# Kernel tuning notes

Measured on AMD Instinct MI355X. Metric: run time of the kernel, lower is better.

The kernel has to match this reference:

```python
import jax, jax.numpy as jnp
import numpy as np

B, S, PATCH_DIM, TRANS_DIM, POS_HID = 16, 4096, 384, 384, 128
SCALE = TRANS_DIM ** (-0.5)

def gelu(x):
    return jax.nn.gelu(x, approximate=False)  # torch nn.GELU default = exact erf

def setup_inputs() -> dict:
    key = jax.random.key(0)
    ks = jax.random.split(key, 16)
    def lin(k, fan_in, shape):
        bound = 1.0 / np.sqrt(fan_in)
        return jax.random.uniform(k, shape, jnp.float32, -bound, bound)
    return {
        "idx": 0,
        "q": jax.random.normal(ks[0], (B, S, TRANS_DIM), jnp.float32),
        "x": jax.random.normal(ks[1], (B, S, 3 + PATCH_DIM), jnp.float32),
        "W_pos1": lin(ks[2], 3, (3, POS_HID)),
        "b_pos1": lin(ks[3], 3, (POS_HID,)),
        "W_pos2": lin(ks[4], POS_HID, (POS_HID, TRANS_DIM)),
        "b_pos2": lin(ks[5], POS_HID, (TRANS_DIM,)),
        "W_in": lin(ks[6], PATCH_DIM, (PATCH_DIM, TRANS_DIM)),
        "b_in": lin(ks[7], PATCH_DIM, (TRANS_DIM,)),
        "W_q": lin(ks[8], TRANS_DIM, (TRANS_DIM, TRANS_DIM)),
        "W_k": lin(ks[9], TRANS_DIM, (TRANS_DIM, TRANS_DIM)),
        "W_v": lin(ks[10], TRANS_DIM, (TRANS_DIM, TRANS_DIM)),
        "W_g1": lin(ks[11], TRANS_DIM, (TRANS_DIM, TRANS_DIM)),
        "b_g1": lin(ks[12], TRANS_DIM, (TRANS_DIM,)),
        "W_g2": lin(ks[13], TRANS_DIM, (TRANS_DIM, TRANS_DIM)),
        "b_g2": lin(ks[14], TRANS_DIM, (TRANS_DIM,)),
        "W_out": lin(ks[15], TRANS_DIM, (TRANS_DIM, PATCH_DIM)),
        "b_out": jnp.zeros((PATCH_DIM,), jnp.float32),
    }

def reference(idx, q, x, W_pos1, b_pos1, W_pos2, b_pos2, W_in, b_in,
              W_q, W_k, W_v, W_g1, b_g1, W_g2, b_g2, W_out, b_out):
    centroid = x[:, :, :3]          # [B,S,3]
    pre = x[:, :, 3:]               # [B,S,patch_dim]
    pos_emb = gelu(centroid @ W_pos1 + b_pos1) @ W_pos2 + b_pos2
    h = pre @ W_in + b_in + pos_emb  # [B,S,trans_dim]
    # idx == 0 path: q = w_qs(h)
    q_out = h @ W_q
    k = h @ W_k
    v = h @ W_v
    gate = gelu((q_out - k) @ W_g1 + b_g1) @ W_g2 + b_g2
    attn = jax.nn.softmax(gate * SCALE, axis=-1)  # softmax over channel dim
    res = (attn * v) @ W_out + b_out + pre
    return (q_out, res)
```

## Files before the change

### kernel.cpp

```cpp
#include <hip/hip_runtime.h>


#define NTOK   65536
#define DIMS   384
#define XC     387
#define TM     32
#define LDP    392
#define PHP    136
#define SCALE  0.051031036307982884f
#define WS_WEIGHT_ELEMS 1081344
#define WS_FLAG_OFF     (WS_WEIGHT_ELEMS)

typedef __bf16 bf16x8 __attribute__((ext_vector_type(8)));
typedef float  floatx4 __attribute__((ext_vector_type(4)));

__device__ __forceinline__ float bf2f(ushort u) {
    return __uint_as_float(((unsigned)u) << 16);
}
__device__ __forceinline__ ushort f2bf(float f) {
    unsigned u = __float_as_uint(f);
    unsigned r = (u + 0x7FFFu + ((u >> 16) & 1u)) >> 16;
    return (ushort)r;
}
__device__ __forceinline__ float gelu_f(float v) {
    return 0.5f * v * (1.0f + erff(v * 0.70710678118654752f));
}
__device__ __forceinline__ float ldg(const void* p, size_t i, int isbf) {
    return isbf ? bf2f(((const ushort*)p)[i]) : ((const float*)p)[i];
}
__device__ __forceinline__ void stg(void* p, size_t i, float v, int isbf) {
    if (isbf) ((ushort*)p)[i] = f2bf(v);
    else      ((float*)p)[i]  = v;
}

__global__ void detect_dtype(const ushort* x, int* flag) {
    int ok = 1;
    for (int i = threadIdx.x; i < 256; i += 64) {
        ushort u = x[2 * i];
        int e = (u >> 7) & 0xFF;
        if (!(e == 0 || (e >= 90 && e <= 141))) ok = 0;
    }
    unsigned long long m = __ballot(ok);
    if (threadIdx.x == 0) *flag = (m == ~0ULL) ? 1 : 0;
}

__global__ void prep_weights(
    const void* __restrict__ Wpos2, const void* __restrict__ Win,
    const void* __restrict__ Wq,    const void* __restrict__ Wk,
    const void* __restrict__ Wv,    const void* __restrict__ Wg1,
    const void* __restrict__ Wg2,   const void* __restrict__ Wo,
    ushort* __restrict__ ws, const int* __restrict__ flagp)
{
    const int isbf = *flagp;
    const int nt   = blockIdx.x;
    const int y    = blockIdx.y;
    const int lane = threadIdx.x;
    const void* src;
    int kt, KT; size_t dstoff;
    if (y < 4) { src = Wpos2; KT = 4; kt = y; dstoff = 0; }
    else {
        int wi = (y - 4) / 12; kt = (y - 4) % 12; KT = 12;
        const void* tab[7] = {Win, Wq, Wk, Wv, Wg1, Wg2, Wo};
        src = tab[wi];
        dstoff = 49152 + (size_t)wi * 147456;
    }
    const int k = kt * 32 + (lane >> 4) * 8;
    const int n = nt * 16 + (lane & 15);
    ushort* dst = ws + dstoff + ((size_t)(nt * KT + kt) * 64 + lane) * 8;
    if (isbf) {
        const ushort* s16 = (const ushort*)src;
#pragma unroll
        for (int j = 0; j < 8; ++j) dst[j] = s16[(size_t)(k + j) * 384 + n];
    } else {
        const float* s32 = (const float*)src;
#pragma unroll
        for (int j = 0; j < 8; ++j) dst[j] = f2bf(s32[(size_t)(k + j) * 384 + n]);
    }
}

template<int KT, int LDA>
__device__ __forceinline__ void gemm_acc(const ushort* sA, const bf16x8* wq,
                                         int ntBase, int lane, floatx4 acc[2][3])
{
    const int l16 = lane & 15, quad = lane >> 4;
#pragma unroll
    for (int kt = 0; kt < KT; ++kt) {
        const int k = kt * 32 + quad * 8;
        bf16x8 a[2];
#pragma unroll
        for (int mt = 0; mt < 2; ++mt)
            a[mt] = *reinterpret_cast<const bf16x8*>(sA + (mt * 16 + l16) * LDA + k);
        bf16x8 b[3];
#pragma unroll
        for (int i = 0; i < 3; ++i)
            b[i] = wq[((size_t)(ntBase + i) * KT + kt) * 64 + lane];
#pragma unroll
        for (int mt = 0; mt < 2; ++mt)
#pragma unroll
            for (int i = 0; i < 3; ++i)
                acc[mt][i] = __builtin_amdgcn_mfma_f32_16x16x32_bf16(a[mt], b[i], acc[mt][i], 0, 0, 0);
    }
}

__device__ __forceinline__ void zero_acc(floatx4 acc[2][3]) {
#pragma unroll
    for (int mt = 0; mt < 2; ++mt)
#pragma unroll
        for (int i = 0; i < 3; ++i)
            acc[mt][i] = (floatx4){0.f, 0.f, 0.f, 0.f};
}

__device__ __forceinline__ void bias_acc(floatx4 acc[2][3], const void* b,
                                         int ntBase, int l16, int isbf) {
#pragma unroll
    for (int i = 0; i < 3; ++i) {
        float bv = ldg(b, (ntBase + i) * 16 + l16, isbf);
#pragma unroll
        for (int mt = 0; mt < 2; ++mt) acc[mt][i] = (floatx4){bv, bv, bv, bv};
    }
}

__device__ __forceinline__ void store_lds(ushort* buf, floatx4 acc[2][3],
                                          int quad, int l16, int ntBase, bool dog) {
#pragma unroll
    for (int mt = 0; mt < 2; ++mt)
#pragma unroll
        for (int i = 0; i < 3; ++i)
#pragma unroll
            for (int r = 0; r < 4; ++r) {
                int rowl = mt * 16 + quad * 4 + r;
                int col  = (ntBase + i) * 16 + l16;
                float v = acc[mt][i][r];
                if (dog) v = gelu_f(v);
                buf[rowl * LDP + col] = f2bf(v);
            }
}

__global__ __launch_bounds__(512, 4) void fused_kernel(
    const void* __restrict__ x,
    const void* __restrict__ Wpos1, const void* __restrict__ bpos1,
    const void* __restrict__ bpos2, const void* __restrict__ bin,
    const void* __restrict__ bg1,   const void* __restrict__ bg2,
    const void* __restrict__ bout,
    const ushort* __restrict__ wpack,
    void* __restrict__ out, const int* __restrict__ flagp)
{
    __shared__ __align__(16) ushort bufA[TM * LDP];
    __shared__ __align__(16) ushort bufB[TM * LDP];
    __shared__ float  cent[TM * 4];
    __shared__ float  rowsum[TM];

    const int isbf   = *flagp;
    const int tid    = (int)threadIdx.x;
    const int lane   = tid & 63;
    const int w      = tid >> 6;
    const int l16    = lane & 15;
    const int quad   = lane >> 4;
    const int ntBase = w * 3;
    const int row0   = (int)blockIdx.x * TM;

    const bf16x8* wq      = reinterpret_cast<const bf16x8*>(wpack);
    const bf16x8* wq_pos2 = wq;
    const bf16x8* wq_in   = wq + 6144;
    const bf16x8* wq_q    = wq + 24576;
    const bf16x8* wq_k    = wq + 43008;
    const bf16x8* wq_v    = wq + 61440;
    const bf16x8* wq_g1   = wq + 79872;
    const bf16x8* wq_g2   = wq + 98304;
    const bf16x8* wq_o    = wq + 116736;

    if (isbf) {
        const ushort* xp = (const ushort*)x;
        for (int idx = tid; idx < TM * DIMS; idx += 512) {
            int m = idx / DIMS, c = idx - m * DIMS;
            bufA[m * LDP + c] = xp[(size_t)(row0 + m) * XC + 3 + c];
        }
    } else {
        const float* xp = (const float*)x;
        for (int idx = tid; idx < TM * DIMS; idx += 512) {
            int m = idx / DIMS, c = idx - m * DIMS;
            bufA[m * LDP + c] = f2bf(xp[(size_t)(row0 + m) * XC + 3 + c]);
        }
    }
    if (tid < TM * 3) {
        int m = tid / 3, j = tid - m * 3;
        cent[m * 4 + j] = ldg(x, (size_t)(row0 + m) * XC + j, isbf);
    }
    if (tid < TM) rowsum[tid] = 0.f;
    __syncthreads();

    for (int idx = tid; idx < TM * 128; idx += 512) {
        int m = idx >> 7, c = idx & 127;
        float a = ldg(bpos1, c, isbf)
                + cent[m * 4 + 0] * ldg(Wpos1, c,       isbf)
                + cent[m * 4 + 1] * ldg(Wpos1, 128 + c, isbf)
                + cent[m * 4 + 2] * ldg(Wpos1, 256 + c, isbf);
        bufB[m * PHP + c] = f2bf(gelu_f(a));
    }
    __syncthreads();

    floatx4 acc[2][3];

#pragma unroll
    for (int mt = 0; mt < 2; ++mt)
#pragma unroll
        for (int i = 0; i < 3; ++i) {
            int col = (ntBase + i) * 16 + l16;
            float bv = ldg(bin, col, isbf) + ldg(bpos2, col, isbf);
            acc[mt][i] = (floatx4){bv, bv, bv, bv};
        }
    gemm_acc<12, LDP>(bufA, wq_in,   ntBase, lane, acc);
    gemm_acc<4,  PHP>(bufB, wq_pos2, ntBase, lane, acc);
    __syncthreads();
    store_lds(bufA, acc, quad, l16, ntBase, false);
    __syncthreads();

    zero_acc(acc);
    gemm_acc<12, LDP>(bufA, wq_k, ntBase, lane, acc);
    store_lds(bufB, acc, quad, l16, ntBase, false);
    __syncthreads();

    zero_acc(acc);
    gemm_acc<12, LDP>(bufA, wq_q, ntBase, lane, acc);
#pragma unroll
    for (int mt = 0; mt < 2; ++mt)
#pragma unroll
        for (int i = 0; i < 3; ++i)
#pragma unroll
            for (int r = 0; r < 4; ++r) {
                int rowl = mt * 16 + quad * 4 + r;
                int col  = (ntBase + i) * 16 + l16;
                float qv = acc[mt][i][r];
                stg(out, (size_t)(row0 + rowl) * DIMS + col, qv, isbf);
                int o = rowl * LDP + col;
                float kv = bf2f(bufB[o]);
                bufB[o] = f2bf(qv - kv);
            }
    __syncthreads();

    zero_acc(acc);
    gemm_acc<12, LDP>(bufA, wq_v, ntBase, lane, acc);
    unsigned vpk[2][3][2];
#pragma unroll
    for (int mt = 0; mt < 2; ++mt)
#pragma unroll
        for (int i = 0; i < 3; ++i) {
            vpk[mt][i][0] = (unsigned)f2bf(acc[mt][i][0]) | ((unsigned)f2bf(acc[mt][i][1]) << 16);
            vpk[mt][i][1] = (unsigned)f2bf(acc[mt][i][2]) | ((unsigned)f2bf(acc[mt][i][3]) << 16);
        }
    __syncthreads();

    bias_acc(acc, bg1, ntBase, l16, isbf);
    gemm_acc<12, LDP>(bufB, wq_g1, ntBase, lane, acc);
    store_lds(bufA, acc, quad, l16, ntBase, true);
    __syncthreads();

    bias_acc(acc, bg2, ntBase, l16, isbf);
    gemm_acc<12, LDP>(bufA, wq_g2, ntBase, lane, acc);
#pragma unroll
    for (int mt = 0; mt < 2; ++mt)
#pragma unroll
        for (int r = 0; r < 4; ++r) {
            float p = 0.f;
#pragma unroll
            for (int i = 0; i < 3; ++i) {
                float e = __expf(acc[mt][i][r] * SCALE);
                acc[mt][i][r] = e;
                p += e;
            }
#pragma unroll
            for (int msk = 1; msk < 16; msk <<= 1) p += __shfl_xor(p, msk, 64);
            if (l16 == 0) atomicAdd(&rowsum[mt * 16 + quad * 4 + r], p);
        }
    __syncthreads();
#pragma unroll
    for (int mt = 0; mt < 2; ++mt)
#pragma unroll
        for (int r = 0; r < 4; ++r) {
            int rowl = mt * 16 + quad * 4 + r;
            float inv = 1.f / rowsum[rowl];
#pragma unroll
            for (int i = 0; i < 3; ++i) {
                int col = (ntBase + i) * 16 + l16;
                float vv = bf2f((ushort)(vpk[mt][i][r >> 1] >> ((r & 1) * 16)));
                bufA[rowl * LDP + col] = f2bf(acc[mt][i][r] * inv * vv);
            }
        }
    __syncthreads();

    bias_acc(acc, bout, ntBase, l16, isbf);
    gemm_acc<12, LDP>(bufA, wq_o, ntBase, lane, acc);
#pragma unroll
    for (int mt = 0; mt < 2; ++mt)
#pragma unroll
        for (int i = 0; i < 3; ++i)
#pragma unroll
            for (int r = 0; r < 4; ++r) {
                int rowl = mt * 16 + quad * 4 + r;
                int col  = (ntBase + i) * 16 + l16;
                size_t tok = (size_t)(row0 + rowl);
                float pre = ldg(x, tok * XC + 3 + col, isbf);
                stg(out, (size_t)NTOK * DIMS + tok * DIMS + col,
                    acc[mt][i][r] + pre, isbf);
            }
}

extern "C" void kernel_launch(void* const* d_in, const int* in_sizes, int n_in,
                              void* d_out, int out_size, void* d_ws, size_t ws_size,
                              hipStream_t stream) {
    const void* x     = d_in[2];
    const void* Wpos1 = d_in[3];
    const void* bpos1 = d_in[4];
    const void* Wpos2 = d_in[5];
    const void* bpos2 = d_in[6];
    const void* Win   = d_in[7];
    const void* bin   = d_in[8];
    const void* Wq    = d_in[9];
    const void* Wk    = d_in[10];
    const void* Wv    = d_in[11];
    const void* Wg1   = d_in[12];
    const void* bg1   = d_in[13];
    const void* Wg2   = d_in[14];
    const void* bg2   = d_in[15];
    const void* Wo    = d_in[16];
    const void* bout  = d_in[17];
    ushort* ws  = (ushort*)d_ws;
    int* flag   = (int*)(ws + WS_FLAG_OFF);

    detect_dtype<<<1, 64, 0, stream>>>((const ushort*)x, flag);

    dim3 pgrid(24, 88);
    prep_weights<<<pgrid, 64, 0, stream>>>(Wpos2, Win, Wq, Wk, Wv, Wg1, Wg2, Wo, ws, flag);

    fused_kernel<<<dim3(NTOK / TM), 512, 0, stream>>>(
        x, Wpos1, bpos1, bpos2, bin, bg1, bg2, bout, ws, d_out, flag);
}
```

Before: 559.8 us.

## Fuse Q/K/V projections into one MFMA pass and use tanh-form GELU

Merges the three separate Q, K and V GEMMs into a single loop, so each LDS A-fragment is loaded once and feeds three sets of accumulators. This also removes two barriers and the LDS round trip of K. The exact erf GELU is replaced with the tanh-form approximation written as x*sigmoid. The bf16 conversion now uses the compiler builtin. Occupancy hints drop from 4 to 2 blocks per CU to leave room for the tripled accumulator registers, at the cost of fewer resident waves and a small numerical deviation from exact GELU.

```diff
diff --git a/kernel.cpp b/kernel.cpp
--- a/kernel.cpp
+++ b/kernel.cpp
@@ -18,12 +18,13 @@
     return __uint_as_float(((unsigned)u) << 16);
 }
 __device__ __forceinline__ ushort f2bf(float f) {
-    unsigned u = __float_as_uint(f);
-    unsigned r = (u + 0x7FFFu + ((u >> 16) & 1u)) >> 16;
-    return (ushort)r;
+    return __builtin_bit_cast(unsigned short, static_cast<__bf16>(f));
 }
 __device__ __forceinline__ float gelu_f(float v) {
-    return 0.5f * v * (1.0f + erff(v * 0.70710678118654752f));
+    float u = 1.5957691216057308f * v * (1.0f + 0.044715f * v * v);
+    u = fminf(u, 64.0f);
+    float e = __expf(u);
+    return v * __fdividef(e, e + 1.0f);
 }
 __device__ __forceinline__ float ldg(const void* p, size_t i, int isbf) {
     return isbf ? bf2f(((const ushort*)p)[i]) : ((const float*)p)[i];
@@ -102,6 +103,38 @@
     }
 }
 
+__device__ __forceinline__ void gemm_qkv(const ushort* sA,
+                                         const bf16x8* wqq, const bf16x8* wqk, const bf16x8* wqv,
+                                         int ntBase, int lane,
+                                         floatx4 aq[2][3], floatx4 ak[2][3], floatx4 av[2][3])
+{
+    const int l16 = lane & 15, quad = lane >> 4;
+#pragma unroll
+    for (int kt = 0; kt < 12; ++kt) {
+        const int k = kt * 32 + quad * 8;
+        bf16x8 a[2];
+#pragma unroll
+        for (int mt = 0; mt < 2; ++mt)
+            a[mt] = *reinterpret_cast<const bf16x8*>(sA + (mt * 16 + l16) * LDP + k);
+        bf16x8 bq[3], bk[3], bv[3];
+#pragma unroll
+        for (int i = 0; i < 3; ++i) {
+            size_t qi = ((size_t)(ntBase + i) * 12 + kt) * 64 + lane;
+            bq[i] = wqq[qi];
+            bk[i] = wqk[qi];
+            bv[i] = wqv[qi];
+        }
+#pragma unroll
+        for (int mt = 0; mt < 2; ++mt)
+#pragma unroll
+            for (int i = 0; i < 3; ++i) {
+                aq[mt][i] = __builtin_amdgcn_mfma_f32_16x16x32_bf16(a[mt], bq[i], aq[mt][i], 0, 0, 0);
+                ak[mt][i] = __builtin_amdgcn_mfma_f32_16x16x32_bf16(a[mt], bk[i], ak[mt][i], 0, 0, 0);
+                av[mt][i] = __builtin_amdgcn_mfma_f32_16x16x32_bf16(a[mt], bv[i], av[mt][i], 0, 0, 0);
+            }
+    }
+}
+
 __device__ __forceinline__ void zero_acc(floatx4 acc[2][3]) {
 #pragma unroll
     for (int mt = 0; mt < 2; ++mt)
@@ -136,7 +169,7 @@
             }
 }
 
-__global__ __launch_bounds__(512, 4) void fused_kernel(
+__global__ __launch_bounds__(512, 2) void fused_kernel(
     const void* __restrict__ x,
     const void* __restrict__ Wpos1, const void* __restrict__ bpos1,
     const void* __restrict__ bpos2, const void* __restrict__ bin,
@@ -187,8 +220,8 @@
         cent[m * 4 + j] = ldg(x, (size_t)(row0 + m) * XC + j, isbf);
     }
     if (tid < TM) rowsum[tid] = 0.f;
-    __syncthreads();
-
+
+    __syncthreads();
     for (int idx = tid; idx < TM * 128; idx += 512) {
         int m = idx >> 7, c = idx & 127;
         float a = ldg(bpos1, c, isbf)
@@ -215,38 +248,24 @@
     store_lds(bufA, acc, quad, l16, ntBase, false);
     __syncthreads();
 
-    zero_acc(acc);
-    gemm_acc<12, LDP>(bufA, wq_k, ntBase, lane, acc);
-    store_lds(bufB, acc, quad, l16, ntBase, false);
-    __syncthreads();
-
-    zero_acc(acc);
-    gemm_acc<12, LDP>(bufA, wq_q, ntBase, lane, acc);
-#pragma unroll
-    for (int mt = 0; mt < 2; ++mt)
-#pragma unroll
-        for (int i = 0; i < 3; ++i)
+    floatx4 aq[2][3], ak[2][3], av[2][3];
+    zero_acc(aq); zero_acc(ak); zero_acc(av);
+    gemm_qkv(bufA, wq_q, wq_k, wq_v, ntBase, lane, aq, ak, av);
+    unsigned vpk[2][3][2];
+#pragma unroll
+    for (int mt = 0; mt < 2; ++mt)
+#pragma unroll
+        for (int i = 0; i < 3; ++i) {
 #pragma unroll
             for (int r = 0; r < 4; ++r) {
                 int rowl = mt * 16 + quad * 4 + r;
                 int col  = (ntBase + i) * 16 + l16;
-                float qv = acc[mt][i][r];
+                float qv = aq[mt][i][r];
                 stg(out, (size_t)(row0 + rowl) * DIMS + col, qv, isbf);
-                int o = rowl * LDP + col;
-                float kv = bf2f(bufB[o]);
-                bufB[o] = f2bf(qv - kv);
-            }
-    __syncthreads();
-
-    zero_acc(acc);
-    gemm_acc<12, LDP>(bufA, wq_v, ntBase, lane, acc);
-    unsigned vpk[2][3][2];
-#pragma unroll
-    for (int mt = 0; mt < 2; ++mt)
-#pragma unroll
-        for (int i = 0; i < 3; ++i) {
-            vpk[mt][i][0] = (unsigned)f2bf(acc[mt][i][0]) | ((unsigned)f2bf(acc[mt][i][1]) << 16);
-            vpk[mt][i][1] = (unsigned)f2bf(acc[mt][i][2]) | ((unsigned)f2bf(acc[mt][i][3]) << 16);
+                bufB[rowl * LDP + col] = f2bf(qv - ak[mt][i][r]);
+            }
+            vpk[mt][i][0] = (unsigned)f2bf(av[mt][i][0]) | ((unsigned)f2bf(av[mt][i][1]) << 16);
+            vpk[mt][i][1] = (unsigned)f2bf(av[mt][i][2]) | ((unsigned)f2bf(av[mt][i][3]) << 16);
         }
     __syncthreads();
 
@@ -283,13 +302,13 @@
             for (int i = 0; i < 3; ++i) {
                 int col = (ntBase + i) * 16 + l16;
                 float vv = bf2f((ushort)(vpk[mt][i][r >> 1] >> ((r & 1) * 16)));
-                bufA[rowl * LDP + col] = f2bf(acc[mt][i][r] * inv * vv);
+                bufB[rowl * LDP + col] = f2bf(acc[mt][i][r] * inv * vv);
             }
         }
     __syncthreads();
 
     bias_acc(acc, bout, ntBase, l16, isbf);
-    gemm_acc<12, LDP>(bufA, wq_o, ntBase, lane, acc);
+    gemm_acc<12, LDP>(bufB, wq_o, ntBase, lane, acc);
 #pragma unroll
     for (int mt = 0; mt < 2; ++mt)
 #pragma unroll
```

Result: slower. 666.2 us (+19.0%).

## Double-buffer GEMM operand loads and use tanh-approx GELU and native bf16 conversion

Applied to the files above, without the earlier changes.

Restructures the MFMA GEMM inner loop into a two-stage software pipeline so the next k-tile's A and B fragments load while the current tile's MFMAs run. Replaces exact erf GELU with the tanh approximation written as a sigmoid through a fast exponential. Replaces the manual float-to-bf16 rounding with the compiler's native conversion. The approximation changes numerics slightly relative to the exact-erf reference, and the extra fragment buffers increase register pressure.

```diff
diff --git a/kernel.cpp b/kernel.cpp
--- a/kernel.cpp
+++ b/kernel.cpp
@@ -18,12 +18,13 @@
     return __uint_as_float(((unsigned)u) << 16);
 }
 __device__ __forceinline__ ushort f2bf(float f) {
-    unsigned u = __float_as_uint(f);
-    unsigned r = (u + 0x7FFFu + ((u >> 16) & 1u)) >> 16;
-    return (ushort)r;
+    return __builtin_bit_cast(unsigned short, static_cast<__bf16>(f));
 }
 __device__ __forceinline__ float gelu_f(float v) {
-    return 0.5f * v * (1.0f + erff(v * 0.70710678118654752f));
+    float u = 1.5957691216057308f * v * (1.0f + 0.044715f * v * v);
+    u = fminf(u, 64.0f);
+    float e = __expf(u);
+    return v * __fdividef(e, e + 1.0f);
 }
 __device__ __forceinline__ float ldg(const void* p, size_t i, int isbf) {
     return isbf ? bf2f(((const ushort*)p)[i]) : ((const float*)p)[i];
@@ -82,23 +83,34 @@
 __device__ __forceinline__ void gemm_acc(const ushort* sA, const bf16x8* wq,
                                          int ntBase, int lane, floatx4 acc[2][3])
 {
+    static_assert(KT % 2 == 0, "KT must be even for 2-stage pipeline");
     const int l16 = lane & 15, quad = lane >> 4;
-#pragma unroll
-    for (int kt = 0; kt < KT; ++kt) {
+    const bf16x8* wp = wq + (size_t)ntBase * KT * 64 + lane;
+    bf16x8 a0[2], a1[2], b0[3], b1[3];
+    auto ldB = [&](bf16x8* b, int kt) {
+#pragma unroll
+        for (int i = 0; i < 3; ++i) b[i] = wp[((size_t)i * KT + kt) * 64];
+    };
+    auto ldA = [&](bf16x8* a, int kt) {
         const int k = kt * 32 + quad * 8;
-        bf16x8 a[2];
 #pragma unroll
         for (int mt = 0; mt < 2; ++mt)
             a[mt] = *reinterpret_cast<const bf16x8*>(sA + (mt * 16 + l16) * LDA + k);
-        bf16x8 b[3];
-#pragma unroll
-        for (int i = 0; i < 3; ++i)
-            b[i] = wq[((size_t)(ntBase + i) * KT + kt) * 64 + lane];
+    };
+    auto mm = [&](bf16x8* a, bf16x8* b) {
 #pragma unroll
         for (int mt = 0; mt < 2; ++mt)
 #pragma unroll
             for (int i = 0; i < 3; ++i)
                 acc[mt][i] = __builtin_amdgcn_mfma_f32_16x16x32_bf16(a[mt], b[i], acc[mt][i], 0, 0, 0);
+    };
+    ldB(b0, 0); ldA(a0, 0);
+#pragma unroll
+    for (int kt = 0; kt < KT; kt += 2) {
+        ldB(b1, kt + 1); ldA(a1, kt + 1);
+        mm(a0, b0);
+        if (kt + 2 < KT) { ldB(b0, kt + 2); ldA(a0, kt + 2); }
+        mm(a1, b1);
     }
 }
 
```

Result: no change. 567.1 us (+1.3%).
